# Performance work log

Measured on AMD Instinct MI355X. Metric: run time of the kernel, lower is better.

The kernel has to match this reference:

```python
import jax, jax.numpy as jnp
import numpy as np


def setup_inputs() -> dict:
    key = jax.random.key(0)
    k_x, k_q, k_k, k_v = jax.random.split(key, 4)
    B, S, F, U = 8, 2048, 1024, 256
    x = jax.random.normal(k_x, (B, S, F), dtype=jnp.float32)
    Wq = jax.random.normal(k_q, (F, U), dtype=jnp.float32) * 0.05
    Wk = jax.random.normal(k_k, (F, U), dtype=jnp.float32) * 0.05
    Wv = jax.random.normal(k_v, (F, U), dtype=jnp.float32) * 0.05
    return {"x": x, "Wq": Wq, "Wk": Wk, "Wv": Wv}


def reference(x, Wq, Wk, Wv):
    # x: [B, S, F]; projections tanh-activated: [B, S, U]
    xQ = jnp.tanh(jnp.einsum("bsf,fu->bsu", x, Wq))
    xK = jnp.tanh(jnp.einsum("bsf,fu->bsu", x, Wk))
    xV = jnp.tanh(jnp.einsum("bsf,fu->bsu", x, Wv))
    scale = 1.0 / jnp.sqrt(jnp.asarray(x.shape[-1], dtype=jnp.float32))
    scores = jnp.einsum("bsu,btu->bst", xQ, xK) * scale  # [B, S, S]
    weights = jax.nn.softmax(scores, axis=-1)
    out = jnp.einsum("bst,btu->bsu", weights, xV)  # return_sequences=True
    return out
```

## Files before the change

### kernel.cpp

```cpp
#include <hip/hip_runtime.h>
#include <math.h>

#define B_ 8
#define S_ 2048
#define F_ 1024
#define U_ 256
#define M_ (B_ * S_)

typedef __attribute__((ext_vector_type(8))) short bf16x8;
typedef __attribute__((ext_vector_type(4))) float f32x4;
typedef __attribute__((ext_vector_type(16))) float f32x16;
typedef unsigned short ushort_t;

__device__ __forceinline__ unsigned short f2bf(float x) {
    unsigned u = __builtin_bit_cast(unsigned, x);
    unsigned r = (u + 0x7fffu + ((u >> 16) & 1u)) >> 16;
    return (unsigned short)r;
}
__device__ __forceinline__ float bf2f(unsigned short b) {
    return __builtin_bit_cast(float, ((unsigned)b) << 16);
}
__device__ __forceinline__ void gload16(const void* g, void* l) {
    __builtin_amdgcn_global_load_lds(
        (const __attribute__((address_space(1))) unsigned int*)g,
        (__attribute__((address_space(3))) unsigned int*)l, 16, 0, 0);
}
__device__ __forceinline__ f32x4 zero4() {
    f32x4 v; v[0] = 0.f; v[1] = 0.f; v[2] = 0.f; v[3] = 0.f; return v;
}

__global__ __launch_bounds__(256) void convxt_kernel(
    const float* __restrict__ x, ushort_t* __restrict__ xbt)
{
    __shared__ ushort_t T[8][129][8];

    const int t  = threadIdx.x;
    const int r0 = blockIdx.x * 128;
    const int k0 = blockIdx.y * 64;

    #pragma unroll
    for (int i = 0; i < 8; ++i) {
        const int r = i * 16 + (t >> 4);
        const int c = (t & 15) * 4;
        const float4 v = *reinterpret_cast<const float4*>(
            x + (size_t)(r0 + r) * F_ + k0 + c);
        ushort4 o;
        o.x = f2bf(v.x); o.y = f2bf(v.y); o.z = f2bf(v.z); o.w = f2bf(v.w);
        *reinterpret_cast<ushort4*>(&T[c >> 3][r][c & 7]) = o;
    }
    __syncthreads();
    #pragma unroll
    for (int i = 0; i < 4; ++i) {
        const int ci  = i * 256 + t;
        const int ksl = ci >> 7, r = ci & 127;
        ushort_t* dst = xbt + ((size_t)(blockIdx.y * 8 + ksl) * M_ + r0 + r) * 8;
        *reinterpret_cast<bf16x8*>(dst) =
            *reinterpret_cast<const bf16x8*>(&T[ksl][r][0]);
    }
}

__global__ __launch_bounds__(256) void convw_kernel(
    const float* __restrict__ Wq, const float* __restrict__ Wk,
    const float* __restrict__ Wv, ushort_t* __restrict__ Wp)
{
    const int ks   = blockIdx.x;
    const int wsel = blockIdx.y;
    const float* __restrict__ W = (wsel == 0) ? Wq : (wsel == 1) ? Wk : Wv;
    const int n = threadIdx.x;

    bf16x8 hv, lv;
    #pragma unroll
    for (int j = 0; j < 8; ++j) {
        float v = W[(size_t)(ks * 8 + j) * U_ + n];
        ushort_t h = f2bf(v);
        hv[j] = (short)h;
        lv[j] = (short)f2bf(v - bf2f(h));
    }
    size_t base = (size_t)wsel * 524288;
    *reinterpret_cast<bf16x8*>(&Wp[base + ((size_t)ks) * 2048 + n * 8]) = hv;
    *reinterpret_cast<bf16x8*>(&Wp[base + ((size_t)(128 + ks)) * 2048 + n * 8]) = lv;
}

__global__ __launch_bounds__(256, 3) void proj_mfma_kernel(
    const ushort_t* __restrict__ xbt,
    const ushort_t* __restrict__ Wp,
    ushort_t* __restrict__ qh_g, ushort_t* __restrict__ kh_g,
    ushort_t* __restrict__ vth_g)
{
    __shared__ ushort_t As[2][4 * 128 * 8];
    __shared__ ushort_t Bs[2][2 * 4 * 128 * 8];

    const int orig = blockIdx.x;
    const int xcd  = orig & 7;
    const int i    = orig >> 3;
    const int rt6  = i / 6;
    const int sub  = i - rt6 * 6;
    const int wsel = sub >> 1;
    const int nh   = sub & 1;
    const int row0 = (xcd * 16 + rt6) * 128;
    const int col0 = nh * 128;

    const int tid = threadIdx.x;
    const int l = tid & 63, w = tid >> 6;
    const int wy = w >> 1, wx = w & 1;
    const int m = l & 31, hi = l >> 5;

    const ushort_t* __restrict__ WpB = Wp + (size_t)wsel * 524288;

    f32x16 acc[2][2];
    #pragma unroll
    for (int mr = 0; mr < 2; ++mr)
        #pragma unroll
        for (int nf = 0; nf < 2; ++nf)
            #pragma unroll
            for (int r = 0; r < 16; ++r) acc[mr][nf][r] = 0.f;

    auto stageA = [&](int buf, int ks) {
        #pragma unroll
        for (int it = 0; it < 2; ++it) {
            const int ci = it * 256 + tid;
            const int ksl = ci >> 7, r = ci & 127;
            const ushort_t* src =
                xbt + ((size_t)(ks * 4 + ksl) * M_ + row0 + r) * 8;
            gload16(src, (char*)&As[buf][0] + (size_t)(it * 256 + w * 64) * 16);
        }
    };
    auto stageB = [&](int buf, int ks) {
        #pragma unroll
        for (int it = 0; it < 4; ++it) {
            const int ci = it * 256 + tid;
            const int half = ci >> 9, ksl = (ci >> 7) & 3, n = ci & 127;
            const ushort_t* src = WpB + (size_t)half * 262144
                                  + (size_t)(ks * 4 + ksl) * 2048
                                  + (size_t)(col0 + n) * 8;
            gload16(src, (char*)&Bs[buf][0] + (size_t)(it * 256 + w * 64) * 16);
        }
    };

    stageA(0, 0);
    stageB(0, 0);
    __syncthreads();

    for (int ks = 0; ks < 32; ++ks) {
        const int cur = ks & 1;
        if (ks < 31) { stageA(cur ^ 1, ks + 1); stageB(cur ^ 1, ks + 1); }

        const ushort_t* Ac = &As[cur][0];
        const ushort_t* Bc = &Bs[cur][0];

        #pragma unroll
        for (int g = 0; g < 2; ++g) {
            const int ksl = g * 2 + hi;
            bf16x8 ah[2];
            #pragma unroll
            for (int mr = 0; mr < 2; ++mr)
                ah[mr] = *reinterpret_cast<const bf16x8*>(
                    &Ac[(size_t)(ksl * 128 + wy * 64 + mr * 32 + m) * 8]);
            bf16x8 bh[2], bl[2];
            #pragma unroll
            for (int nf = 0; nf < 2; ++nf) {
                const int nn = wx * 64 + nf * 32 + m;
                bh[nf] = *reinterpret_cast<const bf16x8*>(
                    &Bc[(size_t)(ksl * 128 + nn) * 8]);
                bl[nf] = *reinterpret_cast<const bf16x8*>(
                    &Bc[(size_t)(512 * 8 + (ksl * 128 + nn) * 8)]);
            }
            #pragma unroll
            for (int nf = 0; nf < 2; ++nf)
                #pragma unroll
                for (int mr = 0; mr < 2; ++mr)
                    acc[mr][nf] = __builtin_amdgcn_mfma_f32_32x32x16_bf16(
                        ah[mr], bh[nf], acc[mr][nf], 0, 0, 0);
            #pragma unroll
            for (int nf = 0; nf < 2; ++nf)
                #pragma unroll
                for (int mr = 0; mr < 2; ++mr)
                    acc[mr][nf] = __builtin_amdgcn_mfma_f32_32x32x16_bf16(
                        ah[mr], bl[nf], acc[mr][nf], 0, 0, 0);
        }
        __syncthreads();
    }

    #pragma unroll
    for (int mr = 0; mr < 2; ++mr) {
        const int row_base = row0 + wy * 64 + mr * 32;
        if (wsel < 2) {
            ushort_t* __restrict__ hp = (wsel == 0) ? qh_g : kh_g;
            #pragma unroll
            for (int nf = 0; nf < 2; ++nf) {
                const int u = col0 + wx * 64 + nf * 32 + m;
                #pragma unroll
                for (int reg = 0; reg < 16; ++reg) {
                    const int rl = (reg & 3) + 8 * (reg >> 2) + 4 * hi;
                    hp[(size_t)(row_base + rl) * U_ + u] =
                        f2bf(tanhf(acc[mr][nf][reg]));
                }
            }
        } else {
            const int b     = row0 >> 11;
            const int s_blk = (row0 & 2047) + wy * 64 + mr * 32;
            #pragma unroll
            for (int nf = 0; nf < 2; ++nf) {
                const int u = col0 + wx * 64 + nf * 32 + m;
                #pragma unroll
                for (int rg = 0; rg < 4; ++rg) {
                    ushort4 hv;
                    hv.x = f2bf(tanhf(acc[mr][nf][rg * 4 + 0]));
                    hv.y = f2bf(tanhf(acc[mr][nf][rg * 4 + 1]));
                    hv.z = f2bf(tanhf(acc[mr][nf][rg * 4 + 2]));
                    hv.w = f2bf(tanhf(acc[mr][nf][rg * 4 + 3]));
                    size_t off = ((size_t)b * U_ + u) * S_ + s_blk + 8 * rg + 4 * hi;
                    *reinterpret_cast<ushort4*>(&vth_g[off]) = hv;
                }
            }
        }
    }
}

__global__ __launch_bounds__(256, 2) void attn_mfma_kernel(
    const ushort_t* __restrict__ qh_g,
    const ushort_t* __restrict__ kh_g,
    const ushort_t* __restrict__ vth_g,
    float* __restrict__ O0, float* __restrict__ O1,
    float* __restrict__ ml)
{
    __shared__ ushort_t Kbuf[2][32 * 256];
    __shared__ ushort_t Vbuf[2][256 * 40];
    __shared__ ushort_t Pbuf[4][512];

    const int tid = threadIdx.x;
    const int l  = tid & 63, w = tid >> 6;
    const int kq = l & 15,  g = l >> 4;

    const int logical = (blockIdx.x & 7) * 64 + (blockIdx.x >> 3);
    const int b     = logical >> 6;
    const int qb    = (logical >> 1) & 31;
    const int khalf = logical & 1;
    const int qrow0 = b * S_ + qb * 64 + w * 16;
    const int kb0   = khalf * 1024;

    bf16x8 qh[8];
    {
        const ushort_t* qbh = qh_g + (size_t)(qrow0 + kq) * U_;
        #pragma unroll
        for (int us = 0; us < 8; ++us)
            qh[us] = *reinterpret_cast<const bf16x8*>(qbh + us * 32 + g * 8);
    }

    f32x4 O[16];
    #pragma unroll
    for (int nt = 0; nt < 16; ++nt) O[nt] = zero4();
    float m_run = -INFINITY, l_run = 0.f;

    auto stage = [&](int buf, int k0) {
        #pragma unroll
        for (int i = 0; i < 4; ++i) {
            int c = w * 256 + i * 64 + l;
            int key = c >> 5, uc = c & 31;
            int ucs = uc ^ (key & 7);
            size_t so = (size_t)(b * S_ + k0 + key) * U_ + ucs * 8;
            gload16(kh_g + so, &Kbuf[buf][(w * 256 + i * 64) * 8]);
        }
        #pragma unroll
        for (int i = 0; i < 5; ++i) {
            int c = w * 320 + i * 64 + l;
            int u = (c * 52429) >> 18;
            int kc = c - u * 5;
            size_t so = ((size_t)b * U_ + u) * S_ + k0 + kc * 8;
            const ushort_t* sh = (kc < 4) ? (vth_g + so) : vth_g;
            gload16(sh, &Vbuf[buf][(w * 320 + i * 64) * 8]);
        }
    };

    stage(0, kb0);

    const float scale = 0.03125f;

    for (int t = 0; t < 32; ++t) {
        const int cur = t & 1;
        asm volatile("s_waitcnt vmcnt(0)" ::: "memory");
        __builtin_amdgcn_s_barrier();
        if (t < 31) stage(cur ^ 1, kb0 + (t + 1) * 32);

        const ushort_t* Kh = Kbuf[cur];
        const ushort_t* Vh = Vbuf[cur];

        f32x4 hh0 = zero4(), hh1 = zero4();
        #pragma unroll
        for (int us = 0; us < 8; ++us) {
            int off0 = kq * 256 + ((us * 32 + g * 8) ^ ((kq & 7) * 8));
            bf16x8 k0h = *reinterpret_cast<const bf16x8*>(Kh + off0);
            hh0 = __builtin_amdgcn_mfma_f32_16x16x32_bf16(k0h, qh[us], hh0, 0, 0, 0);
            int off1 = off0 + 16 * 256;
            bf16x8 k1h = *reinterpret_cast<const bf16x8*>(Kh + off1);
            hh1 = __builtin_amdgcn_mfma_f32_16x16x32_bf16(k1h, qh[us], hh1, 0, 0, 0);
        }
        f32x4 s0 = hh0 * scale;
        f32x4 s1 = hh1 * scale;

        float tm = fmaxf(fmaxf(fmaxf(s0[0], s0[1]), fmaxf(s0[2], s0[3])),
                         fmaxf(fmaxf(s1[0], s1[1]), fmaxf(s1[2], s1[3])));
        tm = fmaxf(tm, __shfl_xor(tm, 16));
        tm = fmaxf(tm, __shfl_xor(tm, 32));
        const bool defer = __all(tm - m_run <= 4.0f);
        float mn, f;
        if (defer) {
            mn = m_run;
        } else {
            mn = fmaxf(m_run, tm);
            f = __expf(m_run - mn);
            m_run = mn;
        }
        ushort_t ph0[4], ph1[4];
        float su = 0.f;
        #pragma unroll
        for (int r = 0; r < 4; ++r) {
            ph0[r] = f2bf(__expf(s0[r] - mn)); su += bf2f(ph0[r]);
        }
        #pragma unroll
        for (int r = 0; r < 4; ++r) {
            ph1[r] = f2bf(__expf(s1[r] - mn)); su += bf2f(ph1[r]);
        }
        su += __shfl_xor(su, 16);
        su += __shfl_xor(su, 32);

        {
            ushort4 a, c;
            a.x = ph0[0]; a.y = ph0[1]; a.z = ph0[2]; a.w = ph0[3];
            c.x = ph1[0]; c.y = ph1[1]; c.z = ph1[2]; c.w = ph1[3];
            int pw0 = ((g >> 1)) * 128 + kq * 8 + (g & 1) * 4;
            int pw1 = (2 + (g >> 1)) * 128 + kq * 8 + (g & 1) * 4;
            *reinterpret_cast<ushort4*>(&Pbuf[w][pw0]) = a;
            *reinterpret_cast<ushort4*>(&Pbuf[w][pw1]) = c;
        }

        if (defer) {
            l_run += su;
        } else {
            l_run = l_run * f + su;
            float fr0 = __shfl(f, g * 4 + 0), fr1 = __shfl(f, g * 4 + 1);
            float fr2 = __shfl(f, g * 4 + 2), fr3 = __shfl(f, g * 4 + 3);
            #pragma unroll
            for (int nt = 0; nt < 16; ++nt) {
                O[nt][0] *= fr0; O[nt][1] *= fr1;
                O[nt][2] *= fr2; O[nt][3] *= fr3;
            }
        }

        bf16x8 pa_h = *reinterpret_cast<const bf16x8*>(&Pbuf[w][g * 128 + kq * 8]);
        #pragma unroll
        for (int nt = 0; nt < 16; ++nt) {
            int vo = (nt * 16 + kq) * 40 + g * 8;
            bf16x8 vh = *reinterpret_cast<const bf16x8*>(Vh + vo);
            O[nt] = __builtin_amdgcn_mfma_f32_16x16x32_bf16(pa_h, vh, O[nt], 0, 0, 0);
        }
    }

    float* __restrict__ Op = khalf ? O1 : O0;
    #pragma unroll
    for (int nt = 0; nt < 16; ++nt) {
        const int col = nt * 16 + kq;
        Op[(size_t)(qrow0 + g * 4 + 0) * U_ + col] = O[nt][0];
        Op[(size_t)(qrow0 + g * 4 + 1) * U_ + col] = O[nt][1];
        Op[(size_t)(qrow0 + g * 4 + 2) * U_ + col] = O[nt][2];
        Op[(size_t)(qrow0 + g * 4 + 3) * U_ + col] = O[nt][3];
    }
    if (g == 0) {
        ml[((size_t)khalf * M_ + qrow0 + kq) * 2 + 0] = m_run;
        ml[((size_t)khalf * M_ + qrow0 + kq) * 2 + 1] = l_run;
    }
}

__global__ __launch_bounds__(256) void merge_kernel(
    const float* __restrict__ O1, const float* __restrict__ ml,
    float* __restrict__ out)
{
    const int tid = threadIdx.x;
    const int row = blockIdx.x * 4 + (tid >> 6);
    const int c   = (tid & 63) * 4;

    const float m0 = ml[(size_t)row * 2 + 0];
    const float l0 = ml[(size_t)row * 2 + 1];
    const float m1 = ml[((size_t)M_ + row) * 2 + 0];
    const float l1 = ml[((size_t)M_ + row) * 2 + 1];
    const float Mx = fmaxf(m0, m1);
    float a0 = expf(m0 - Mx), a1 = expf(m1 - Mx);
    const float inv = 1.f / (a0 * l0 + a1 * l1);
    a0 *= inv; a1 *= inv;

    const size_t off = (size_t)row * U_ + c;
    const float4 o0 = *reinterpret_cast<const float4*>(out + off);
    const float4 o1 = *reinterpret_cast<const float4*>(O1 + off);
    float4 r;
    r.x = o0.x * a0 + o1.x * a1;
    r.y = o0.y * a0 + o1.y * a1;
    r.z = o0.z * a0 + o1.z * a1;
    r.w = o0.w * a0 + o1.w * a1;
    *reinterpret_cast<float4*>(out + off) = r;
}

extern "C" void kernel_launch(void* const* d_in, const int* in_sizes, int n_in,
                              void* d_out, int out_size, void* d_ws, size_t ws_size,
                              hipStream_t stream)
{
    (void)in_sizes; (void)n_in; (void)out_size; (void)ws_size;
    const float* x  = (const float*)d_in[0];
    const float* Wq = (const float*)d_in[1];
    const float* Wk = (const float*)d_in[2];
    const float* Wv = (const float*)d_in[3];
    float* out = (float*)d_out;

    ushort_t* ws = (ushort_t*)d_ws;
    const size_t T = (size_t)M_ * U_;
    ushort_t* qh_g  = ws;
    ushort_t* kh_g  = ws + T;
    ushort_t* vth_g = ws + 2 * T;
    ushort_t* Wp    = ws + 3 * T;
    ushort_t* xbt   = ws + 3 * T + 1572864;
    float*    O1    = (float*)xbt;
    float*    ml    = O1 + T;

    convxt_kernel<<<dim3(128, 16), 256, 0, stream>>>(x, xbt);
    convw_kernel<<<dim3(128, 3), 256, 0, stream>>>(Wq, Wk, Wv, Wp);

    proj_mfma_kernel<<<dim3(768), 256, 0, stream>>>(
        xbt, Wp, qh_g, kh_g, vth_g);

    attn_mfma_kernel<<<dim3(512), 256, 0, stream>>>(
        qh_g, kh_g, vth_g, out, O1, ml);

    merge_kernel<<<dim3(M_ / 4), 256, 0, stream>>>(O1, ml, out);
}
```

Baseline: 160.2 us.

## Switch attention to 32x32 MFMA tiles with configurable key split

```diff
diff --git a/kernel.cpp b/kernel.cpp
--- a/kernel.cpp
+++ b/kernel.cpp
@@ -24,9 +24,6 @@
     __builtin_amdgcn_global_load_lds(
         (const __attribute__((address_space(1))) unsigned int*)g,
         (__attribute__((address_space(3))) unsigned int*)l, 16, 0, 0);
-}
-__device__ __forceinline__ f32x4 zero4() {
-    f32x4 v; v[0] = 0.f; v[1] = 0.f; v[2] = 0.f; v[3] = 0.f; return v;
 }
 
 __global__ __launch_bounds__(256) void convxt_kernel(
@@ -222,188 +219,206 @@
     const ushort_t* __restrict__ kh_g,
     const ushort_t* __restrict__ vth_g,
     float* __restrict__ O0, float* __restrict__ O1,
-    float* __restrict__ ml)
+    float* __restrict__ ml, int nkh)
 {
     __shared__ ushort_t Kbuf[2][32 * 256];
-    __shared__ ushort_t Vbuf[2][256 * 40];
-    __shared__ ushort_t Pbuf[4][512];
+    __shared__ ushort_t Vbuf[2][256 * 32];
+    __shared__ ushort_t Pbuf[4][32 * 40];
 
     const int tid = threadIdx.x;
     const int l  = tid & 63, w = tid >> 6;
-    const int kq = l & 15,  g = l >> 4;
-
-    const int logical = (blockIdx.x & 7) * 64 + (blockIdx.x >> 3);
-    const int b     = logical >> 6;
-    const int qb    = (logical >> 1) & 31;
-    const int khalf = logical & 1;
-    const int qrow0 = b * S_ + qb * 64 + w * 16;
-    const int kb0   = khalf * 1024;
-
-    bf16x8 qh[8];
+    const int q  = l & 31, hi = l >> 5;
+
+    const int per_b  = 16 * nkh;
+    const int logical = (blockIdx.x & 7) * per_b + (blockIdx.x >> 3);
+    const int b  = logical / per_b;
+    const int r  = logical - b * per_b;
+    const int qt = r / nkh;
+    const int kh = r - qt * nkh;
+    const int ksz = S_ / nkh;
+    const int kb0 = kh * ksz;
+    const int qrow0 = b * S_ + qt * 128 + w * 32;
+
+    bf16x8 qf[16];
     {
-        const ushort_t* qbh = qh_g + (size_t)(qrow0 + kq) * U_;
-        #pragma unroll
-        for (int us = 0; us < 8; ++us)
-            qh[us] = *reinterpret_cast<const bf16x8*>(qbh + us * 32 + g * 8);
-    }
-
-    f32x4 O[16];
-    #pragma unroll
-    for (int nt = 0; nt < 16; ++nt) O[nt] = zero4();
+        const ushort_t* qb = qh_g + (size_t)(qrow0 + q) * U_ + hi * 8;
+        #pragma unroll
+        for (int c = 0; c < 16; ++c)
+            qf[c] = *reinterpret_cast<const bf16x8*>(qb + c * 16);
+    }
+
+    f32x16 O[8];
+    #pragma unroll
+    for (int ut = 0; ut < 8; ++ut)
+        #pragma unroll
+        for (int rg = 0; rg < 16; ++rg) O[ut][rg] = 0.f;
     float m_run = -INFINITY, l_run = 0.f;
 
     auto stage = [&](int buf, int k0) {
         #pragma unroll
         for (int i = 0; i < 4; ++i) {
             int c = w * 256 + i * 64 + l;
-            int key = c >> 5, uc = c & 31;
-            int ucs = uc ^ (key & 7);
-            size_t so = (size_t)(b * S_ + k0 + key) * U_ + ucs * 8;
+            int key = c >> 5, s = c & 31;
+            int ss = s ^ (key & 7);
+            size_t so = (size_t)(b * S_ + k0 + key) * U_ + ss * 8;
             gload16(kh_g + so, &Kbuf[buf][(w * 256 + i * 64) * 8]);
         }
         #pragma unroll
-        for (int i = 0; i < 5; ++i) {
-            int c = w * 320 + i * 64 + l;
-            int u = (c * 52429) >> 18;
-            int kc = c - u * 5;
-            size_t so = ((size_t)b * U_ + u) * S_ + k0 + kc * 8;
-            const ushort_t* sh = (kc < 4) ? (vth_g + so) : vth_g;
-            gload16(sh, &Vbuf[buf][(w * 320 + i * 64) * 8]);
+        for (int i = 0; i < 4; ++i) {
+            int c = w * 256 + i * 64 + l;
+            int u = c >> 2, s = c & 3;
+            int ss = s ^ (u & 3);
+            size_t so = ((size_t)b * U_ + u) * S_ + k0 + ss * 8;
+            gload16(vth_g + so, &Vbuf[buf][(w * 256 + i * 64) * 8]);
         }
     };
 
     stage(0, kb0);
 
     const float scale = 0.03125f;
-
-    for (int t = 0; t < 32; ++t) {
+    const int ntile = ksz / 32;
+
+    for (int t = 0; t < ntile; ++t) {
         const int cur = t & 1;
         asm volatile("s_waitcnt vmcnt(0)" ::: "memory");
         __builtin_amdgcn_s_barrier();
-        if (t < 31) stage(cur ^ 1, kb0 + (t + 1) * 32);
+        if (t < ntile - 1) stage(cur ^ 1, kb0 + (t + 1) * 32);
 
         const ushort_t* Kh = Kbuf[cur];
         const ushort_t* Vh = Vbuf[cur];
 
-        f32x4 hh0 = zero4(), hh1 = zero4();
-        #pragma unroll
-        for (int us = 0; us < 8; ++us) {
-            int off0 = kq * 256 + ((us * 32 + g * 8) ^ ((kq & 7) * 8));
-            bf16x8 k0h = *reinterpret_cast<const bf16x8*>(Kh + off0);
-            hh0 = __builtin_amdgcn_mfma_f32_16x16x32_bf16(k0h, qh[us], hh0, 0, 0, 0);
-            int off1 = off0 + 16 * 256;
-            bf16x8 k1h = *reinterpret_cast<const bf16x8*>(Kh + off1);
-            hh1 = __builtin_amdgcn_mfma_f32_16x16x32_bf16(k1h, qh[us], hh1, 0, 0, 0);
-        }
-        f32x4 s0 = hh0 * scale;
-        f32x4 s1 = hh1 * scale;
-
-        float tm = fmaxf(fmaxf(fmaxf(s0[0], s0[1]), fmaxf(s0[2], s0[3])),
-                         fmaxf(fmaxf(s1[0], s1[1]), fmaxf(s1[2], s1[3])));
-        tm = fmaxf(tm, __shfl_xor(tm, 16));
+        f32x16 Sacc;
+        #pragma unroll
+        for (int rg = 0; rg < 16; ++rg) Sacc[rg] = 0.f;
+        #pragma unroll
+        for (int c = 0; c < 16; ++c) {
+            const int key = q;
+            const int off = key * 256 + (((2 * c + hi) ^ (key & 7)) * 8);
+            bf16x8 kf = *reinterpret_cast<const bf16x8*>(Kh + off);
+            Sacc = __builtin_amdgcn_mfma_f32_32x32x16_bf16(kf, qf[c], Sacc, 0, 0, 0);
+        }
+
+        float tm = Sacc[0] * scale;
+        #pragma unroll
+        for (int rg = 1; rg < 16; ++rg) tm = fmaxf(tm, Sacc[rg] * scale);
         tm = fmaxf(tm, __shfl_xor(tm, 32));
         const bool defer = __all(tm - m_run <= 4.0f);
-        float mn, f;
-        if (defer) {
-            mn = m_run;
-        } else {
+        float mn = m_run, f;
+        if (!defer) {
             mn = fmaxf(m_run, tm);
             f = __expf(m_run - mn);
             m_run = mn;
         }
-        ushort_t ph0[4], ph1[4];
+        ushort_t ph[16];
         float su = 0.f;
         #pragma unroll
-        for (int r = 0; r < 4; ++r) {
-            ph0[r] = f2bf(__expf(s0[r] - mn)); su += bf2f(ph0[r]);
-        }
-        #pragma unroll
-        for (int r = 0; r < 4; ++r) {
-            ph1[r] = f2bf(__expf(s1[r] - mn)); su += bf2f(ph1[r]);
-        }
-        su += __shfl_xor(su, 16);
+        for (int rg = 0; rg < 16; ++rg) {
+            ph[rg] = f2bf(__expf(Sacc[rg] * scale - mn));
+            su += bf2f(ph[rg]);
+        }
         su += __shfl_xor(su, 32);
 
         {
-            ushort4 a, c;
-            a.x = ph0[0]; a.y = ph0[1]; a.z = ph0[2]; a.w = ph0[3];
-            c.x = ph1[0]; c.y = ph1[1]; c.z = ph1[2]; c.w = ph1[3];
-            int pw0 = ((g >> 1)) * 128 + kq * 8 + (g & 1) * 4;
-            int pw1 = (2 + (g >> 1)) * 128 + kq * 8 + (g & 1) * 4;
-            *reinterpret_cast<ushort4*>(&Pbuf[w][pw0]) = a;
-            *reinterpret_cast<ushort4*>(&Pbuf[w][pw1]) = c;
+            ushort_t* pr = &Pbuf[w][q * 40];
+            #pragma unroll
+            for (int grp = 0; grp < 4; ++grp) {
+                ushort4 v;
+                v.x = ph[grp * 4 + 0]; v.y = ph[grp * 4 + 1];
+                v.z = ph[grp * 4 + 2]; v.w = ph[grp * 4 + 3];
+                *reinterpret_cast<ushort4*>(pr + grp * 8 + hi * 4) = v;
+            }
         }
 
         if (defer) {
             l_run += su;
         } else {
             l_run = l_run * f + su;
-            float fr0 = __shfl(f, g * 4 + 0), fr1 = __shfl(f, g * 4 + 1);
-            float fr2 = __shfl(f, g * 4 + 2), fr3 = __shfl(f, g * 4 + 3);
-            #pragma unroll
-            for (int nt = 0; nt < 16; ++nt) {
-                O[nt][0] *= fr0; O[nt][1] *= fr1;
-                O[nt][2] *= fr2; O[nt][3] *= fr3;
-            }
-        }
-
-        bf16x8 pa_h = *reinterpret_cast<const bf16x8*>(&Pbuf[w][g * 128 + kq * 8]);
-        #pragma unroll
-        for (int nt = 0; nt < 16; ++nt) {
-            int vo = (nt * 16 + kq) * 40 + g * 8;
-            bf16x8 vh = *reinterpret_cast<const bf16x8*>(Vh + vo);
-            O[nt] = __builtin_amdgcn_mfma_f32_16x16x32_bf16(pa_h, vh, O[nt], 0, 0, 0);
-        }
-    }
-
-    float* __restrict__ Op = khalf ? O1 : O0;
-    #pragma unroll
-    for (int nt = 0; nt < 16; ++nt) {
-        const int col = nt * 16 + kq;
-        Op[(size_t)(qrow0 + g * 4 + 0) * U_ + col] = O[nt][0];
-        Op[(size_t)(qrow0 + g * 4 + 1) * U_ + col] = O[nt][1];
-        Op[(size_t)(qrow0 + g * 4 + 2) * U_ + col] = O[nt][2];
-        Op[(size_t)(qrow0 + g * 4 + 3) * U_ + col] = O[nt][3];
-    }
-    if (g == 0) {
-        ml[((size_t)khalf * M_ + qrow0 + kq) * 2 + 0] = m_run;
-        ml[((size_t)khalf * M_ + qrow0 + kq) * 2 + 1] = l_run;
+            #pragma unroll
+            for (int rg = 0; rg < 16; ++rg) {
+                const int qv = (rg & 3) + 8 * (rg >> 2) + 4 * hi;
+                const float fr = __shfl(f, qv);
+                #pragma unroll
+                for (int ut = 0; ut < 8; ++ut) O[ut][rg] *= fr;
+            }
+        }
+
+        bf16x8 pf[2];
+        #pragma unroll
+        for (int kc = 0; kc < 2; ++kc)
+            pf[kc] = *reinterpret_cast<const bf16x8*>(
+                &Pbuf[w][q * 40 + kc * 16 + hi * 8]);
+        #pragma unroll
+        for (int ut = 0; ut < 8; ++ut) {
+            #pragma unroll
+            for (int kc = 0; kc < 2; ++kc) {
+                const int u = ut * 32 + q;
+                const int off = u * 32 + (((kc * 2 + hi) ^ (u & 3)) * 8);
+                bf16x8 vf = *reinterpret_cast<const bf16x8*>(Vh + off);
+                O[ut] = __builtin_amdgcn_mfma_f32_32x32x16_bf16(pf[kc], vf, O[ut], 0, 0, 0);
+            }
+        }
+    }
+
+    float* __restrict__ Op = (kh == 0) ? O0 : (O1 + (size_t)(kh - 1) * M_ * U_);
+    #pragma unroll
+    for (int ut = 0; ut < 8; ++ut) {
+        #pragma unroll
+        for (int rg = 0; rg < 16; ++rg) {
+            const int qv = (rg & 3) + 8 * (rg >> 2) + 4 * hi;
+            Op[(size_t)(qrow0 + qv) * U_ + ut * 32 + q] = O[ut][rg];
+        }
+    }
+    if (hi == 0) {
+        ml[((size_t)kh * M_ + qrow0 + q) * 2 + 0] = m_run;
+        ml[((size_t)kh * M_ + qrow0 + q) * 2 + 1] = l_run;
     }
 }
 
 __global__ __launch_bounds__(256) void merge_kernel(
     const float* __restrict__ O1, const float* __restrict__ ml,
-    float* __restrict__ out)
+    float* __restrict__ out, int nkh)
 {
     const int tid = threadIdx.x;
     const int row = blockIdx.x * 4 + (tid >> 6);
     const int c   = (tid & 63) * 4;
 
-    const float m0 = ml[(size_t)row * 2 + 0];
-    const float l0 = ml[(size_t)row * 2 + 1];
-    const float m1 = ml[((size_t)M_ + row) * 2 + 0];
-    const float l1 = ml[((size_t)M_ + row) * 2 + 1];
-    const float Mx = fmaxf(m0, m1);
-    float a0 = expf(m0 - Mx), a1 = expf(m1 - Mx);
-    const float inv = 1.f / (a0 * l0 + a1 * l1);
-    a0 *= inv; a1 *= inv;
+    float mv[4], lv[4];
+    float Mx = -INFINITY;
+    for (int j = 0; j < nkh; ++j) {
+        mv[j] = ml[((size_t)j * M_ + row) * 2 + 0];
+        lv[j] = ml[((size_t)j * M_ + row) * 2 + 1];
+        Mx = fmaxf(Mx, mv[j]);
+    }
+    float denom = 0.f;
+    float a[4];
+    for (int j = 0; j < nkh; ++j) {
+        a[j] = __expf(mv[j] - Mx);
+        denom += a[j] * lv[j];
+    }
+    const float inv = 1.f / denom;
 
     const size_t off = (size_t)row * U_ + c;
-    const float4 o0 = *reinterpret_cast<const float4*>(out + off);
-    const float4 o1 = *reinterpret_cast<const float4*>(O1 + off);
-    float4 r;
-    r.x = o0.x * a0 + o1.x * a1;
-    r.y = o0.y * a0 + o1.y * a1;
-    r.z = o0.z * a0 + o1.z * a1;
-    r.w = o0.w * a0 + o1.w * a1;
-    *reinterpret_cast<float4*>(out + off) = r;
+    float4 racc;
+    {
+        const float4 o0 = *reinterpret_cast<const float4*>(out + off);
+        const float s = a[0] * inv;
+        racc.x = o0.x * s; racc.y = o0.y * s; racc.z = o0.z * s; racc.w = o0.w * s;
+    }
+    for (int j = 1; j < nkh; ++j) {
+        const float4 oj = *reinterpret_cast<const float4*>(
+            O1 + (size_t)(j - 1) * M_ * U_ + off);
+        const float s = a[j] * inv;
+        racc.x += oj.x * s; racc.y += oj.y * s;
+        racc.z += oj.z * s; racc.w += oj.w * s;
+    }
+    *reinterpret_cast<float4*>(out + off) = racc;
 }
 
 extern "C" void kernel_launch(void* const* d_in, const int* in_sizes, int n_in,
                               void* d_out, int out_size, void* d_ws, size_t ws_size,
                               hipStream_t stream)
 {
-    (void)in_sizes; (void)n_in; (void)out_size; (void)ws_size;
+    (void)in_sizes; (void)n_in; (void)out_size;
     const float* x  = (const float*)d_in[0];
     const float* Wq = (const float*)d_in[1];
     const float* Wk = (const float*)d_in[2];
@@ -418,7 +433,8 @@
     ushort_t* Wp    = ws + 3 * T;
     ushort_t* xbt   = ws + 3 * T + 1572864;
     float*    O1    = (float*)xbt;
-    float*    ml    = O1 + T;
+    const int nkh = (ws_size >= 79167488ull) ? 4 : 2;
+    float*    ml    = O1 + (size_t)(nkh - 1) * T;
 
     convxt_kernel<<<dim3(128, 16), 256, 0, stream>>>(x, xbt);
     convw_kernel<<<dim3(128, 3), 256, 0, stream>>>(Wq, Wk, Wv, Wp);
@@ -426,8 +442,8 @@
     proj_mfma_kernel<<<dim3(768), 256, 0, stream>>>(
         xbt, Wp, qh_g, kh_g, vth_g);
 
-    attn_mfma_kernel<<<dim3(512), 256, 0, stream>>>(
-        qh_g, kh_g, vth_g, out, O1, ml);
-
-    merge_kernel<<<dim3(M_ / 4), 256, 0, stream>>>(O1, ml, out);
-}
+    attn_mfma_kernel<<<dim3(128 * nkh), 256, 0, stream>>>(
+        qh_g, kh_g, vth_g, out, O1, ml, nkh);
+
+    merge_kernel<<<dim3(M_ / 4), 256, 0, stream>>>(O1, ml, out, nkh);
+}
```

Measured after the change: 169.2 us. 1.06x slower.

## Use single bf16 pass for Q/K projections, fold score scale into Q

Applied to the files above, without the earlier changes.

```diff
diff --git a/kernel.cpp b/kernel.cpp
--- a/kernel.cpp
+++ b/kernel.cpp
@@ -99,6 +99,7 @@
     const int nh   = sub & 1;
     const int row0 = (xcd * 16 + rt6) * 128;
     const int col0 = nh * 128;
+    const bool twopass = (wsel == 2);
 
     const int tid = threadIdx.x;
     const int l = tid & 63, w = tid >> 6;
@@ -126,8 +127,8 @@
         }
     };
     auto stageB = [&](int buf, int ks) {
-        #pragma unroll
-        for (int it = 0; it < 4; ++it) {
+        const int nit = twopass ? 4 : 2;
+        for (int it = 0; it < nit; ++it) {
             const int ci = it * 256 + tid;
             const int half = ci >> 9, ksl = (ci >> 7) & 3, n = ci & 127;
             const ushort_t* src = WpB + (size_t)half * 262144
@@ -156,14 +157,12 @@
             for (int mr = 0; mr < 2; ++mr)
                 ah[mr] = *reinterpret_cast<const bf16x8*>(
                     &Ac[(size_t)(ksl * 128 + wy * 64 + mr * 32 + m) * 8]);
-            bf16x8 bh[2], bl[2];
+            bf16x8 bh[2];
             #pragma unroll
             for (int nf = 0; nf < 2; ++nf) {
                 const int nn = wx * 64 + nf * 32 + m;
                 bh[nf] = *reinterpret_cast<const bf16x8*>(
                     &Bc[(size_t)(ksl * 128 + nn) * 8]);
-                bl[nf] = *reinterpret_cast<const bf16x8*>(
-                    &Bc[(size_t)(512 * 8 + (ksl * 128 + nn) * 8)]);
             }
             #pragma unroll
             for (int nf = 0; nf < 2; ++nf)
@@ -171,16 +170,26 @@
                 for (int mr = 0; mr < 2; ++mr)
                     acc[mr][nf] = __builtin_amdgcn_mfma_f32_32x32x16_bf16(
                         ah[mr], bh[nf], acc[mr][nf], 0, 0, 0);
-            #pragma unroll
-            for (int nf = 0; nf < 2; ++nf)
+            if (twopass) {
+                bf16x8 bl[2];
                 #pragma unroll
-                for (int mr = 0; mr < 2; ++mr)
-                    acc[mr][nf] = __builtin_amdgcn_mfma_f32_32x32x16_bf16(
-                        ah[mr], bl[nf], acc[mr][nf], 0, 0, 0);
+                for (int nf = 0; nf < 2; ++nf) {
+                    const int nn = wx * 64 + nf * 32 + m;
+                    bl[nf] = *reinterpret_cast<const bf16x8*>(
+                        &Bc[(size_t)(512 * 8 + (ksl * 128 + nn) * 8)]);
+                }
+                #pragma unroll
+                for (int nf = 0; nf < 2; ++nf)
+                    #pragma unroll
+                    for (int mr = 0; mr < 2; ++mr)
+                        acc[mr][nf] = __builtin_amdgcn_mfma_f32_32x32x16_bf16(
+                            ah[mr], bl[nf], acc[mr][nf], 0, 0, 0);
+            }
         }
         __syncthreads();
     }
 
+    const float oscale = (wsel == 0) ? 0.03125f : 1.0f;
     #pragma unroll
     for (int mr = 0; mr < 2; ++mr) {
         const int row_base = row0 + wy * 64 + mr * 32;
@@ -193,7 +202,7 @@
                 for (int reg = 0; reg < 16; ++reg) {
                     const int rl = (reg & 3) + 8 * (reg >> 2) + 4 * hi;
                     hp[(size_t)(row_base + rl) * U_ + u] =
-                        f2bf(tanhf(acc[mr][nf][reg]));
+                        f2bf(tanhf(acc[mr][nf][reg]) * oscale);
                 }
             }
         } else {
@@ -274,8 +283,6 @@
 
     stage(0, kb0);
 
-    const float scale = 0.03125f;
-
     for (int t = 0; t < 32; ++t) {
         const int cur = t & 1;
         asm volatile("s_waitcnt vmcnt(0)" ::: "memory");
@@ -285,28 +292,24 @@
         const ushort_t* Kh = Kbuf[cur];
         const ushort_t* Vh = Vbuf[cur];
 
-        f32x4 hh0 = zero4(), hh1 = zero4();
+        f32x4 s0 = zero4(), s1 = zero4();
         #pragma unroll
         for (int us = 0; us < 8; ++us) {
             int off0 = kq * 256 + ((us * 32 + g * 8) ^ ((kq & 7) * 8));
             bf16x8 k0h = *reinterpret_cast<const bf16x8*>(Kh + off0);
-            hh0 = __builtin_amdgcn_mfma_f32_16x16x32_bf16(k0h, qh[us], hh0, 0, 0, 0);
+            s0 = __builtin_amdgcn_mfma_f32_16x16x32_bf16(k0h, qh[us], s0, 0, 0, 0);
             int off1 = off0 + 16 * 256;
             bf16x8 k1h = *reinterpret_cast<const bf16x8*>(Kh + off1);
-            hh1 = __builtin_amdgcn_mfma_f32_16x16x32_bf16(k1h, qh[us], hh1, 0, 0, 0);
-        }
-        f32x4 s0 = hh0 * scale;
-        f32x4 s1 = hh1 * scale;
+            s1 = __builtin_amdgcn_mfma_f32_16x16x32_bf16(k1h, qh[us], s1, 0, 0, 0);
+        }
 
         float tm = fmaxf(fmaxf(fmaxf(s0[0], s0[1]), fmaxf(s0[2], s0[3])),
                          fmaxf(fmaxf(s1[0], s1[1]), fmaxf(s1[2], s1[3])));
         tm = fmaxf(tm, __shfl_xor(tm, 16));
         tm = fmaxf(tm, __shfl_xor(tm, 32));
         const bool defer = __all(tm - m_run <= 4.0f);
-        float mn, f;
-        if (defer) {
-            mn = m_run;
-        } else {
+        float mn = m_run, f;
+        if (!defer) {
             mn = fmaxf(m_run, tm);
             f = __expf(m_run - mn);
             m_run = mn;
@@ -384,7 +387,7 @@
     const float m1 = ml[((size_t)M_ + row) * 2 + 0];
     const float l1 = ml[((size_t)M_ + row) * 2 + 1];
     const float Mx = fmaxf(m0, m1);
-    float a0 = expf(m0 - Mx), a1 = expf(m1 - Mx);
+    float a0 = __expf(m0 - Mx), a1 = __expf(m1 - Mx);
     const float inv = 1.f / (a0 * l0 + a1 * l1);
     a0 *= inv; a1 *= inv;
 
```

New measurement: 146.8 us, median of 4. 8.3% less time.
